# Optimization experiments

Measured on AMD Instinct MI355X. Metric: run time of the kernel, lower is better.

Reference implementation:

```python
import jax, jax.numpy as jnp
import numpy as np

N_HIDDEN = 96
N_LAYER = 4
IN_FEAT = 24


def _lstm_layer(xs, W_ih, W_hh, b):
    # xs: [T, B, in]; W_ih: [4H, in]; W_hh: [4H, H]; b: [4H]
    B = xs.shape[1]
    h0 = jnp.zeros((B, N_HIDDEN), xs.dtype)
    c0 = jnp.zeros((B, N_HIDDEN), xs.dtype)

    def step(carry, x_t):
        h, c = carry
        gates = x_t @ W_ih.T + h @ W_hh.T + b  # [B, 4H], torch gate order i,f,g,o
        i, f, g, o = jnp.split(gates, 4, axis=-1)
        i = jax.nn.sigmoid(i)
        f = jax.nn.sigmoid(f)
        g = jnp.tanh(g)
        o = jax.nn.sigmoid(o)
        c = f * c + i * g
        h = o * jnp.tanh(c)
        return (h, c), h

    (hT, cT), ys = jax.lax.scan(step, (h0, c0), xs)
    return ys, hT


def setup_inputs() -> dict:
    key = jax.random.key(0)
    ks = jax.random.split(key, 16)
    B, T = 4096, 128
    k = 1.0 / np.sqrt(N_HIDDEN)  # torch default LSTM init bound
    u = lambda kk, shape: jax.random.uniform(kk, shape, jnp.float32, -k, k)
    inp = {
        "x": jax.random.normal(ks[0], (B, T, IN_FEAT), jnp.float32),
        "W_ih0": u(ks[1], (4 * N_HIDDEN, IN_FEAT)),          # layer 0 input weights
        "W_ih_rest": u(ks[2], (N_LAYER - 1, 4 * N_HIDDEN, N_HIDDEN)),  # layers 1..3
        "W_hh": u(ks[3], (N_LAYER, 4 * N_HIDDEN, N_HIDDEN)),
        "b_ih": u(ks[4], (N_LAYER, 4 * N_HIDDEN)),
        "b_hh": u(ks[5], (N_LAYER, 4 * N_HIDDEN)),
        "fc1_w": u(ks[6], (16, N_HIDDEN)),
        "fc1_b": u(ks[7], (16,)),
        "fc2_w": u(ks[8], (8, 16)),
        "fc2_b": u(ks[9], (8,)),
        "fc3_w": u(ks[10], (1, 8)),
        "fc3_b": u(ks[11], (1,)),
    }
    return inp


def reference(x, W_ih0, W_ih_rest, W_hh, b_ih, b_hh,
              fc1_w, fc1_b, fc2_w, fc2_b, fc3_w, fc3_b):
    # x: [B, T, F] (batch_first); scan over time -> [T, B, F]
    xs = jnp.transpose(x, (1, 0, 2))
    hns = []
    ys, h = _lstm_layer(xs, W_ih0, W_hh[0], b_ih[0] + b_hh[0])
    hns.append(h)
    for l in range(N_LAYER - 1):  # inter-layer dropout p=0.1 -> identity in eval
        ys, h = _lstm_layer(ys, W_ih_rest[l], W_hh[l + 1], b_ih[l + 1] + b_hh[l + 1])
        hns.append(h)
    # original forward detaches hn via numpy round-trip -> stop_gradient
    hn_sum = jax.lax.stop_gradient(hns[-1] + hns[1])  # [B, H]
    z = jax.nn.relu(hn_sum)
    z = jax.nn.relu(z @ fc1_w.T + fc1_b)
    z = jax.nn.relu(z @ fc2_w.T + fc2_b)
    out = z @ fc3_w.T + fc3_b  # head dropout p=0.1 -> identity in eval
    return out  # [B, 1]
```

## Files before the change

kernel.cpp:

```cpp
#include <hip/hip_runtime.h>
#include <math.h>

typedef _Float16 f16;
typedef _Float16 f16x8 __attribute__((ext_vector_type(8)));
typedef float f32x4 __attribute__((ext_vector_type(4)));
typedef float f32x2 __attribute__((ext_vector_type(2)));

#define B_TOTAL 4096
#define T_STEPS 128
#define H 96
#define NB 16
#define NTH 768
#define NBLK (B_TOTAL/NB)
#define ST_T (NB*H)
#define LOG2E 1.44269504088896f

__device__ __forceinline__ float sig2(float vp){
    return __builtin_amdgcn_rcpf(1.f + __builtin_amdgcn_exp2f(-vp));
}
__device__ __forceinline__ float tanh2(float vpp){
    return 1.f - 2.f*__builtin_amdgcn_rcpf(__builtin_amdgcn_exp2f(vpp) + 1.f);
}
__device__ __forceinline__ float tanh_c(float c){
    return tanh2(c * (2.f*LOG2E));
}

__device__ __forceinline__ void lds_barrier(){
    __builtin_amdgcn_sched_barrier(0);
    asm volatile("s_waitcnt lgkmcnt(0)" ::: "memory");
    __builtin_amdgcn_s_barrier();
    __builtin_amdgcn_sched_barrier(0);
}

template<int F, bool IS_L0, bool HAS_YSOUT, bool WRITE_HSUM, bool ADD_HSUM>
__device__ __forceinline__ void layer_run(
    const float* __restrict__ x32, f16* __restrict__ strip,
    const float* __restrict__ Wi, const float* __restrict__ Wh,
    const float* __restrict__ bi, const float* __restrict__ bh,
    f16* sh, f16* sl, float* p_lds, float* hsum, int row0)
{
    constexpr int  KS   = (F + H + 31)/32;
    constexpr int  KP   = KS*32;
    constexpr int  KPB  = KP*2;
    constexpr bool HAS_LO = IS_L0;
    constexpr int  BUF  = 16*KP;

    const int tid=threadIdx.x, lane=tid&63, w=tid>>6;
    const int j15=lane&15, g4=lane>>4;
    const int g=w>>1;
    const int qsel=w&1;
    const int u=16*g+j15;
    const int sr=tid/48, su=(tid-sr*48)*2;
    const int ysrd_off = sr*KPB + (((F+su)*2) ^ ((sr&7)<<4));

    for (int i=tid;i<2*BUF;i+=NTH) sh[i]=(f16)0.f;
    if constexpr (HAS_LO)
        for (int i=tid;i<2*BUF;i+=NTH) sl[i]=(f16)0.f;

    f16x8 Bf[2][KS];
    float scl[2];
#pragma unroll
    for (int qq=0;qq<2;++qq){
        int qg = qsel + 2*qq;
        scl[qq] = (qg==2) ? 2.f*LOG2E : LOG2E;
    }
#pragma unroll
    for (int qq=0;qq<2;++qq){
        const int j=96*(qsel+2*qq)+u;
#pragma unroll
        for (int s=0;s<KS;++s){
            f16x8 f;
#pragma unroll
            for (int e=0;e<8;++e){
                int k=32*s+8*g4+e;
                float v=0.f;
                if (k<F)        v=Wi[(size_t)j*F+k];
                else if (k-F<H) v=Wh[(size_t)j*H+(k-F)];
                f[e]=(f16)(v*scl[qq]);
            }
            Bf[qq][s]=f;
        }
    }
    float bq[2];
#pragma unroll
    for (int qq=0;qq<2;++qq)
        bq[qq]=(bi[96*(qsel+2*qq)+u]+bh[96*(qsel+2*qq)+u])*scl[qq];

    float c4[4]={0.f,0.f,0.f,0.f};

    unsigned*       ysst = (unsigned*)strip + tid;
    const unsigned* yld  = (const unsigned*)strip + (ST_T/2) + tid;
    const int yr=(tid*2)/H, yk=(tid*2)-yr*H;
    const int yoff = yr*KPB + ((yk*2)^((yr&7)<<4));

    const int xr=tid/24, xk=tid-xr*24;
    const bool xact = IS_L0 && (tid < NB*24);
    const float* xbase = xact ? x32 + (size_t)(row0+xr)*(T_STEPS*24) + xk : nullptr;
    const int xoff = xr*KPB + ((xk*2)^((xr&7)<<4));

    if constexpr (IS_L0){
        if (xact){
            float v=xbase[0];
            f16 vh=(f16)v, vl=(f16)(v-(float)vh);
            *(f16*)((char*)sh+xoff)=vh; *(f16*)((char*)sl+xoff)=vl;
        }
    } else {
        unsigned v = *((const unsigned*)strip + tid);
        *(unsigned*)((char*)sh+yoff)=v;
    }
    __syncthreads();

    unsigned yvA=0u;
    if constexpr (!IS_L0){ yvA = *yld; yld += ST_T/2; }

    const int aswz=(j15&7)<<4;
    const int abase=j15*KPB;
    const int pbase = (g*64+lane)*16;
    int nhoB[4], hsiB[4];
#pragma unroll
    for (int r=0;r<4;++r){
        int row=4*g4+r;
        nhoB[r]=row*KPB + (((F+u)*2)^((row&7)<<4));
        hsiB[r]=row*96+u;
    }

#pragma unroll 1
    for (int t=0;t<T_STEPS;++t){
        const int cur=t&1, nxt=cur^1;
        const char* chb=(const char*)(sh+cur*BUF);
        const char* clb=HAS_LO ? (const char*)(sl+cur*BUF) : nullptr;
        char*       nhb=(char*)(sh+nxt*BUF);
        char*       nlb=HAS_LO ? (char*)(sl+nxt*BUF) : nullptr;

        float xv=0.f; unsigned yvB=0u;
        if constexpr (IS_L0){
            if (xact && t+1<T_STEPS) xv = xbase[(size_t)(t+1)*24];
        } else {
            if (t+2<T_STEPS){ yvB = *yld; yld += ST_T/2; }
        }
        __builtin_amdgcn_sched_barrier(0);

        unsigned hbits=0u;
        if (HAS_YSOUT && t>0) hbits = *(const unsigned*)(chb + ysrd_off);

        f32x4 acc[2][2];
#pragma unroll
        for (int qq=0;qq<2;++qq){
            f32x4 a={bq[qq],bq[qq],bq[qq],bq[qq]}; acc[qq][0]=a;
            f32x4 z={0.f,0.f,0.f,0.f};              acc[qq][1]=z;
        }
#pragma unroll
        for (int s=0;s<KS;++s){
            int kb=((s*64+g4*16)^aswz);
            f16x8 ah=*(const f16x8*)(chb+abase+kb);
            if (s&1){
                acc[0][1]=__builtin_amdgcn_mfma_f32_16x16x32_f16(ah,Bf[0][s],acc[0][1],0,0,0);
                acc[1][1]=__builtin_amdgcn_mfma_f32_16x16x32_f16(ah,Bf[1][s],acc[1][1],0,0,0);
            } else {
                acc[0][0]=__builtin_amdgcn_mfma_f32_16x16x32_f16(ah,Bf[0][s],acc[0][0],0,0,0);
                acc[1][0]=__builtin_amdgcn_mfma_f32_16x16x32_f16(ah,Bf[1][s],acc[1][0],0,0,0);
            }
        }
        if constexpr (HAS_LO){
            int kb=((g4*16)^aswz);
            f16x8 al=*(const f16x8*)(clb+abase+kb);
            acc[0][1]=__builtin_amdgcn_mfma_f32_16x16x32_f16(al,Bf[0][0],acc[0][1],0,0,0);
            acc[1][1]=__builtin_amdgcn_mfma_f32_16x16x32_f16(al,Bf[1][0],acc[1][1],0,0,0);
        }

        float af[4], ao[4];
        if (qsel==0){
#pragma unroll
            for (int pr=0;pr<2;++pr){
                float i0=sig2(acc[0][0][2*pr  ]+acc[0][1][2*pr  ]);
                float i1=sig2(acc[0][0][2*pr+1]+acc[0][1][2*pr+1]);
                float g0=tanh2(acc[1][0][2*pr  ]+acc[1][1][2*pr  ]);
                float g1=tanh2(acc[1][0][2*pr+1]+acc[1][1][2*pr+1]);
                f32x2 p={i0*g0, i1*g1};
                *(f32x2*)((char*)p_lds + pbase + pr*8) = p;
            }
        } else {
#pragma unroll
            for (int r=0;r<4;++r){
                af[r]=sig2(acc[0][0][r]+acc[0][1][r]);
                ao[r]=sig2(acc[1][0][r]+acc[1][1][r]);
            }
        }
        lds_barrier();

        if (HAS_YSOUT && t>0){ *ysst = hbits; ysst += ST_T/2; }

        if (qsel==1){
            f32x2 pA = *(const f32x2*)((const char*)p_lds + pbase);
            f32x2 pB = *(const f32x2*)((const char*)p_lds + pbase + 8);
            float p4[4]={pA[0],pA[1],pB[0],pB[1]};
#pragma unroll
            for (int r=0;r<4;++r){
                float c = af[r]*c4[r] + p4[r];
                c4[r]=c;
                float h = ao[r]*tanh_c(c);
                *(f16*)(nhb + nhoB[r]) = (f16)h;
                if constexpr (WRITE_HSUM){ if (t==T_STEPS-1) hsum[hsiB[r]]=h; }
                if constexpr (ADD_HSUM)  { if (t==T_STEPS-1) hsum[hsiB[r]]+=h; }
            }
        }
        if (t+1<T_STEPS){
            if constexpr (IS_L0){
                if (xact){
                    f16 vh=(f16)xv, vl=(f16)(xv-(float)vh);
                    *(f16*)(nhb+xoff)=vh; *(f16*)(nlb+xoff)=vl;
                }
            } else {
                *(unsigned*)(nhb+yoff)=yvA;
            }
        }
        lds_barrier();
        yvA = yvB;
    }
    if constexpr (HAS_YSOUT){
        unsigned hbits = *(const unsigned*)((const char*)sh + ysrd_off);
        asm volatile("s_waitcnt lgkmcnt(0)" ::: "memory");
        *ysst = hbits;
    }
}

__global__ __launch_bounds__(NTH, 1)
void lstm_all(const float* __restrict__ x,
              const float* __restrict__ W_ih0,
              const float* __restrict__ W_ih_rest,
              const float* __restrict__ W_hh,
              const float* __restrict__ b_ih,
              const float* __restrict__ b_hh,
              const float* __restrict__ fc1_w, const float* __restrict__ fc1_b,
              const float* __restrict__ fc2_w, const float* __restrict__ fc2_b,
              const float* __restrict__ fc3_w, const float* __restrict__ fc3_b,
              f16* __restrict__ ws_strip, float* __restrict__ out)
{
    __shared__ f16 sh[2*16*192];
    __shared__ f16 sl[2*16*128];
    __shared__ float p_lds[6*64*4];
    __shared__ float hsum[16*96];
    __shared__ float z1[16*16];
    __shared__ float z2[16*8];

    const int tid=threadIdx.x;
    const int b=blockIdx.x, row0=b*NB;
    f16* strip = ws_strip + (size_t)b*T_STEPS*ST_T;
    const int GH = 384*96;

    layer_run<24, true,  true,  false, false>(x, strip, W_ih0,             W_hh,        b_ih,          b_hh,          sh,sl,p_lds,hsum,row0);
    __syncthreads();
    layer_run<96, false, true,  true,  false>(nullptr, strip, W_ih_rest,        W_hh+1*GH, b_ih+1*384, b_hh+1*384, sh,sl,p_lds,hsum,row0);
    __syncthreads();
    layer_run<96, false, true,  false, false>(nullptr, strip, W_ih_rest+1*GH, W_hh+2*GH, b_ih+2*384, b_hh+2*384, sh,sl,p_lds,hsum,row0);
    __syncthreads();
    layer_run<96, false, false, false, true >(nullptr, strip, W_ih_rest+2*GH, W_hh+3*GH, b_ih+3*384, b_hh+3*384, sh,sl,p_lds,hsum,row0);
    __syncthreads();

    if (tid<256){
        int r=tid>>4, jj=tid&15;
        float a=fc1_b[jj];
        for (int uu=0;uu<96;++uu) a+=fc1_w[jj*96+uu]*fmaxf(hsum[r*96+uu],0.f);
        z1[r*16+jj]=fmaxf(a,0.f);
    }
    __syncthreads();
    if (tid<128){
        int r=tid>>3, jj=tid&7;
        float a=fc2_b[jj];
#pragma unroll
        for (int uu=0;uu<16;++uu) a+=fc2_w[jj*16+uu]*z1[r*16+uu];
        z2[r*8+jj]=fmaxf(a,0.f);
    }
    __syncthreads();
    if (tid<16){
        float a=fc3_b[0];
#pragma unroll
        for (int uu=0;uu<8;++uu) a+=fc3_w[uu]*z2[tid*8+uu];
        out[row0+tid]=a;
    }
}

extern "C" void kernel_launch(void* const* d_in, const int* in_sizes, int n_in,
                              void* d_out, int out_size, void* d_ws, size_t ws_size,
                              hipStream_t stream) {
    const float* x         = (const float*)d_in[0];
    const float* W_ih0     = (const float*)d_in[1];
    const float* W_ih_rest = (const float*)d_in[2];
    const float* W_hh      = (const float*)d_in[3];
    const float* b_ih      = (const float*)d_in[4];
    const float* b_hh      = (const float*)d_in[5];
    const float* fc1_w     = (const float*)d_in[6];
    const float* fc1_b     = (const float*)d_in[7];
    const float* fc2_w     = (const float*)d_in[8];
    const float* fc2_b     = (const float*)d_in[9];
    const float* fc3_w     = (const float*)d_in[10];
    const float* fc3_b     = (const float*)d_in[11];
    float* out = (float*)d_out;

    const size_t WS = (size_t)NBLK * T_STEPS * ST_T * sizeof(f16);
    if (ws_size < WS) {
        hipMemsetAsync(d_out, 0, (size_t)out_size * sizeof(float), stream);
        return;
    }

    lstm_all<<<dim3(NBLK), dim3(NTH), 0, stream>>>(
        x, W_ih0, W_ih_rest, W_hh, b_ih, b_hh,
        fc1_w, fc1_b, fc2_w, fc2_b, fc3_w, fc3_b,
        (f16*)d_ws, out);
}
```

Before: 561.5 us.

## Move strip I/O to gate-i/g waves and prioritize cell-update waves

Reassigns the global strip loads/stores and x staging so that only the qsel==0 waves (which compute i*g) handle them, using 8-byte uint2 accesses instead of 4-byte per-thread accesses across all threads. The qsel==1 waves, which perform the serial cell/hidden update, no longer carry memory traffic and are raised to higher scheduling priority with s_setprio during the update. The p_lds exchange becomes a single 16-byte vector store and load. This aims to shorten the critical path of each recurrent step, at the cost of unbalancing work between the two wave groups.

```diff
diff --git a/kernel.cpp b/kernel.cpp
--- a/kernel.cpp
+++ b/kernel.cpp
@@ -50,8 +50,12 @@
     const int g=w>>1;
     const int qsel=w&1;
     const int u=16*g+j15;
-    const int sr=tid/48, su=(tid-sr*48)*2;
-    const int ysrd_off = sr*KPB + (((F+su)*2) ^ ((sr&7)<<4));
+    const int aidx=(w>>1)*64+lane;
+
+    const int srow=aidx/24, sk0=(aidx-srow*24)*4;
+    const int sswz=(srow&7)<<4;
+    const int ysrd_off = srow*KPB + (((F+sk0)*2) ^ sswz);
+    const int yoffA    = srow*KPB + (((sk0)*2) ^ sswz);
 
     for (int i=tid;i<2*BUF;i+=NTH) sh[i]=(f16)0.f;
     if constexpr (HAS_LO)
@@ -88,34 +92,32 @@
 
     float c4[4]={0.f,0.f,0.f,0.f};
 
-    unsigned*       ysst = (unsigned*)strip + tid;
-    const unsigned* yld  = (const unsigned*)strip + (ST_T/2) + tid;
-    const int yr=(tid*2)/H, yk=(tid*2)-yr*H;
-    const int yoff = yr*KPB + ((yk*2)^((yr&7)<<4));
-
-    const int xr=tid/24, xk=tid-xr*24;
-    const bool xact = IS_L0 && (tid < NB*24);
+    uint2*       ysst2 = (uint2*)strip + aidx;
+    const uint2* yld2  = (const uint2*)strip + (ST_T/4) + aidx;
+
+    const int xr=aidx/24, xk=aidx-xr*24;
+    const bool xact = IS_L0 && (qsel==0);
     const float* xbase = xact ? x32 + (size_t)(row0+xr)*(T_STEPS*24) + xk : nullptr;
     const int xoff = xr*KPB + ((xk*2)^((xr&7)<<4));
 
-    if constexpr (IS_L0){
-        if (xact){
+    if (qsel==0){
+        if constexpr (IS_L0){
             float v=xbase[0];
             f16 vh=(f16)v, vl=(f16)(v-(float)vh);
             *(f16*)((char*)sh+xoff)=vh; *(f16*)((char*)sl+xoff)=vl;
-        }
-    } else {
-        unsigned v = *((const unsigned*)strip + tid);
-        *(unsigned*)((char*)sh+yoff)=v;
-    }
-    __syncthreads();
-
-    unsigned yvA=0u;
-    if constexpr (!IS_L0){ yvA = *yld; yld += ST_T/2; }
+        } else {
+            uint2 v = *((const uint2*)strip + aidx);
+            *(uint2*)((char*)sh+yoffA)=v;
+        }
+    }
+    __syncthreads();
+
+    uint2 yvA2={0u,0u};
+    if (!IS_L0 && qsel==0){ yvA2 = *yld2; yld2 += ST_T/4; }
 
     const int aswz=(j15&7)<<4;
     const int abase=j15*KPB;
-    const int pbase = (g*64+lane)*16;
+    const int pbase=(g*64+lane)*16;
     int nhoB[4], hsiB[4];
 #pragma unroll
     for (int r=0;r<4;++r){
@@ -132,16 +134,17 @@
         char*       nhb=(char*)(sh+nxt*BUF);
         char*       nlb=HAS_LO ? (char*)(sl+nxt*BUF) : nullptr;
 
-        float xv=0.f; unsigned yvB=0u;
+        float xv=0.f; uint2 yvB2={0u,0u};
         if constexpr (IS_L0){
             if (xact && t+1<T_STEPS) xv = xbase[(size_t)(t+1)*24];
         } else {
-            if (t+2<T_STEPS){ yvB = *yld; yld += ST_T/2; }
+            if (qsel==0 && t+2<T_STEPS){ yvB2 = *yld2; yld2 += ST_T/4; }
         }
         __builtin_amdgcn_sched_barrier(0);
 
-        unsigned hbits=0u;
-        if (HAS_YSOUT && t>0) hbits = *(const unsigned*)(chb + ysrd_off);
+        uint2 hbits2={0u,0u};
+        if (HAS_YSOUT && qsel==0 && t>0)
+            hbits2 = *(const uint2*)(chb + ysrd_off);
 
         f32x4 acc[2][2];
 #pragma unroll
@@ -170,15 +173,14 @@
 
         float af[4], ao[4];
         if (qsel==0){
-#pragma unroll
-            for (int pr=0;pr<2;++pr){
-                float i0=sig2(acc[0][0][2*pr  ]+acc[0][1][2*pr  ]);
-                float i1=sig2(acc[0][0][2*pr+1]+acc[0][1][2*pr+1]);
-                float g0=tanh2(acc[1][0][2*pr  ]+acc[1][1][2*pr  ]);
-                float g1=tanh2(acc[1][0][2*pr+1]+acc[1][1][2*pr+1]);
-                f32x2 p={i0*g0, i1*g1};
-                *(f32x2*)((char*)p_lds + pbase + pr*8) = p;
-            }
+            f32x4 p4;
+#pragma unroll
+            for (int r=0;r<4;++r){
+                float iv=sig2(acc[0][0][r]+acc[0][1][r]);
+                float gv=tanh2(acc[1][0][r]+acc[1][1][r]);
+                p4[r]=iv*gv;
+            }
+            *(f32x4*)((char*)p_lds + pbase) = p4;
         } else {
 #pragma unroll
             for (int r=0;r<4;++r){
@@ -188,12 +190,9 @@
         }
         lds_barrier();
 
-        if (HAS_YSOUT && t>0){ *ysst = hbits; ysst += ST_T/2; }
-
         if (qsel==1){
-            f32x2 pA = *(const f32x2*)((const char*)p_lds + pbase);
-            f32x2 pB = *(const f32x2*)((const char*)p_lds + pbase + 8);
-            float p4[4]={pA[0],pA[1],pB[0],pB[1]};
+            __builtin_amdgcn_s_setprio(1);
+            f32x4 p4 = *(const f32x4*)((const char*)p_lds + pbase);
 #pragma unroll
             for (int r=0;r<4;++r){
                 float c = af[r]*c4[r] + p4[r];
@@ -203,24 +202,25 @@
                 if constexpr (WRITE_HSUM){ if (t==T_STEPS-1) hsum[hsiB[r]]=h; }
                 if constexpr (ADD_HSUM)  { if (t==T_STEPS-1) hsum[hsiB[r]]+=h; }
             }
-        }
-        if (t+1<T_STEPS){
-            if constexpr (IS_L0){
-                if (xact){
+            __builtin_amdgcn_s_setprio(0);
+        } else {
+            if (HAS_YSOUT && t>0){ *ysst2 = hbits2; ysst2 += ST_T/4; }
+            if (t+1<T_STEPS){
+                if constexpr (IS_L0){
                     f16 vh=(f16)xv, vl=(f16)(xv-(float)vh);
                     *(f16*)(nhb+xoff)=vh; *(f16*)(nlb+xoff)=vl;
+                } else {
+                    *(uint2*)(nhb+yoffA)=yvA2;
                 }
-            } else {
-                *(unsigned*)(nhb+yoff)=yvA;
             }
         }
         lds_barrier();
-        yvA = yvB;
-    }
-    if constexpr (HAS_YSOUT){
-        unsigned hbits = *(const unsigned*)((const char*)sh + ysrd_off);
+        yvA2 = yvB2;
+    }
+    if (HAS_YSOUT && qsel==0){
+        uint2 hb = *(const uint2*)((const char*)sh + ysrd_off);
         asm volatile("s_waitcnt lgkmcnt(0)" ::: "memory");
-        *ysst = hbits;
+        *ysst2 = hb;
     }
 }
 
```

After: 555.1 us. No clear change (-1.1%).
